# Optimization experiments

Measured on AMD Instinct MI355X. Metric: run time of the kernel, lower is better.

Reference implementation:

```python
import jax, jax.numpy as jnp
import numpy as np

N_VOX, N_COLS = 200000, 5   # (N, 1 + 3 coords + 1 feat)
N_CLUSTS, PTS_PER_CLUST = 1024, 128
N_EDGES = 8192


def setup_inputs() -> dict:
    key = jax.random.key(0)
    k1, k2, k3 = jax.random.split(key, 3)
    data = jax.random.normal(k1, (N_VOX, N_COLS), dtype=jnp.float32)
    clusts = jax.random.randint(k2, (N_CLUSTS, PTS_PER_CLUST), 0, N_VOX)
    edge_index = jax.random.randint(k3, (2, N_EDGES), 0, N_CLUSTS)
    return {"data": data, "clusts": clusts, "edge_index": edge_index}


def reference(data, clusts, edge_index):
    # COORD_COLS = columns 1:4 of the sparse tensor
    voxels = data[:, 1:4]                       # [N, 3]
    pts = voxels[clusts]                        # [C, P, 3]
    x1 = pts[edge_index[0]]                     # [E, P, 3] first cluster of each edge
    x2 = pts[edge_index[1]]                     # [E, P, 3] second cluster
    P = x1.shape[1]

    # per-edge pairwise squared distances (argmin of d^2 == argmin of d)
    d2 = jnp.sum((x1[:, :, None, :] - x2[:, None, :, :]) ** 2, axis=-1)  # [E, P, P]
    imin = jnp.argmin(d2.reshape(d2.shape[0], -1), axis=1)               # [E]
    i1, i2 = imin // P, imin % P

    v1 = jnp.take_along_axis(x1, i1[:, None, None], axis=1)[:, 0, :]     # [E, 3]
    v2 = jnp.take_along_axis(x2, i2[:, None, None], axis=1)[:, 0, :]     # [E, 3]

    disp = v1 - v2
    lend = jnp.linalg.norm(disp, axis=-1, keepdims=True)                 # [E, 1]
    safe = jnp.where(lend > 0, lend, 1.0)
    dispn = jnp.where(lend > 0, disp / safe, disp)                       # unit displacement

    B = (dispn[:, :, None] * dispn[:, None, :]).reshape(-1, 9)           # outer product, [E, 9]

    feats = jnp.concatenate([v1, v2, dispn, lend, B], axis=1)            # [E, 19]
    # undirected: interleave original and flipped (v1<->v2, disp -> -disp, B invariant)
    feats_flip = jnp.concatenate([v2, v1, -dispn, lend, B], axis=1)
    full = jnp.stack([feats, feats_flip], axis=1).reshape(-1, 19)        # [2E, 19]
    return full
```

## Files before the change

### kernel.cpp

```cpp
#include <hip/hip_runtime.h>
#include <cstdint>

#define NV 200000
#define NCOLS 5
#define P 128
#define NE 8192

__global__ __launch_bounds__(256) void clust_geo_edge_kernel(
    const float* __restrict__ data,
    const int*   __restrict__ clusts,
    const int*   __restrict__ edge_index,
    float*       __restrict__ out)
{
    const int e = blockIdx.x;
    const int t = threadIdx.x;

    __shared__ float x1s[P][3];
    __shared__ float x2s[P][3];
    __shared__ unsigned long long wmin[4];

    const int c1 = edge_index[e];
    const int c2 = edge_index[NE + e];

    if (t < P) {
        const int v = clusts[c1 * P + t];
        x1s[t][0] = data[v * NCOLS + 1];
        x1s[t][1] = data[v * NCOLS + 2];
        x1s[t][2] = data[v * NCOLS + 3];
    } else {
        const int p = t - P;
        const int v = clusts[c2 * P + p];
        x2s[p][0] = data[v * NCOLS + 1];
        x2s[p][1] = data[v * NCOLS + 2];
        x2s[p][2] = data[v * NCOLS + 3];
    }
    __syncthreads();

    const int i  = t >> 1;
    const int j0 = (t & 1) * 64;
    const float ax = x1s[i][0], ay = x1s[i][1], az = x1s[i][2];

    float bestd = __builtin_inff();
    int   bestflat = i * P + j0;

    #pragma unroll 8
    for (int k = 0; k < 64; ++k) {
        const int j = j0 + k;
        const float dx = __fsub_rn(ax, x2s[j][0]);
        const float dy = __fsub_rn(ay, x2s[j][1]);
        const float dz = __fsub_rn(az, x2s[j][2]);
        const float d2 = __fadd_rn(__fadd_rn(__fmul_rn(dx, dx), __fmul_rn(dy, dy)),
                                   __fmul_rn(dz, dz));
        if (d2 < bestd) { bestd = d2; bestflat = i * P + j; }
    }

    unsigned long long key =
        ((unsigned long long)__float_as_uint(bestd) << 32) | (unsigned)bestflat;

    for (int off = 32; off > 0; off >>= 1) {
        unsigned long long other = __shfl_down(key, off, 64);
        if (other < key) key = other;
    }
    const int wave = t >> 6;
    if ((t & 63) == 0) wmin[wave] = key;
    __syncthreads();

    if (t == 0) {
        unsigned long long k0 = wmin[0];
        #pragma unroll
        for (int w = 1; w < 4; ++w) if (wmin[w] < k0) k0 = wmin[w];
        const int flat = (int)(k0 & 0xffffffffull);
        const int i1 = flat >> 7;
        const int i2 = flat & (P - 1);

        const float v1x = x1s[i1][0], v1y = x1s[i1][1], v1z = x1s[i1][2];
        const float v2x = x2s[i2][0], v2y = x2s[i2][1], v2z = x2s[i2][2];

        const float dx = v1x - v2x, dy = v1y - v2y, dz = v1z - v2z;
        const float lend = sqrtf(dx * dx + dy * dy + dz * dz);

        float nx, ny, nz;
        if (lend > 0.f) { nx = dx / lend; ny = dy / lend; nz = dz / lend; }
        else            { nx = dx;        ny = dy;        nz = dz;        }

        const float B[9] = { nx*nx, nx*ny, nx*nz,
                             ny*nx, ny*ny, ny*nz,
                             nz*nx, nz*ny, nz*nz };

        float* o = out + (size_t)e * 38;
        o[0] = v1x; o[1] = v1y; o[2] = v1z;
        o[3] = v2x; o[4] = v2y; o[5] = v2z;
        o[6] = nx;  o[7] = ny;  o[8] = nz;  o[9] = lend;
        #pragma unroll
        for (int q = 0; q < 9; ++q) o[10 + q] = B[q];
        o[19] = v2x; o[20] = v2y; o[21] = v2z;
        o[22] = v1x; o[23] = v1y; o[24] = v1z;
        o[25] = -nx; o[26] = -ny; o[27] = -nz; o[28] = lend;
        #pragma unroll
        for (int q = 0; q < 9; ++q) o[29 + q] = B[q];
    }
}

extern "C" void kernel_launch(void* const* d_in, const int* in_sizes, int n_in,
                              void* d_out, int out_size, void* d_ws, size_t ws_size,
                              hipStream_t stream) {
    const float* data       = (const float*)d_in[0];
    const int*   clusts     = (const int*)d_in[1];
    const int*   edge_index = (const int*)d_in[2];
    float*       out        = (float*)d_out;

    clust_geo_edge_kernel<<<NE, 256, 0, stream>>>(data, clusts, edge_index, out);
}
```

Baseline: 98.08 us.

## Register-tile pairwise distance loop 8x8 per thread with float4 shared layout

Each thread now holds 8 points from each cluster in registers and computes an 8x8 block of distances, in place of streaming 64 points from shared memory against a single point. Cluster coordinates are stored padded to float4 so each point can be read from LDS with one vector load. This cuts LDS traffic per distance computation at the cost of more registers and a per-row argmin merge. Ties within a thread are still resolved by lowest flat index, since k increases with i and m increases with j.

```diff
diff --git a/kernel.cpp b/kernel.cpp
--- a/kernel.cpp
+++ b/kernel.cpp
@@ -15,8 +15,8 @@
     const int e = blockIdx.x;
     const int t = threadIdx.x;
 
-    __shared__ float x1s[P][3];
-    __shared__ float x2s[P][3];
+    __shared__ float4 x1s[P];
+    __shared__ float4 x2s[P];
     __shared__ unsigned long long wmin[4];
 
     const int c1 = edge_index[e];
@@ -24,34 +24,50 @@
 
     if (t < P) {
         const int v = clusts[c1 * P + t];
-        x1s[t][0] = data[v * NCOLS + 1];
-        x1s[t][1] = data[v * NCOLS + 2];
-        x1s[t][2] = data[v * NCOLS + 3];
+        x1s[t] = make_float4(data[v * NCOLS + 1], data[v * NCOLS + 2],
+                             data[v * NCOLS + 3], 0.f);
     } else {
         const int p = t - P;
         const int v = clusts[c2 * P + p];
-        x2s[p][0] = data[v * NCOLS + 1];
-        x2s[p][1] = data[v * NCOLS + 2];
-        x2s[p][2] = data[v * NCOLS + 3];
+        x2s[p] = make_float4(data[v * NCOLS + 1], data[v * NCOLS + 2],
+                             data[v * NCOLS + 3], 0.f);
     }
     __syncthreads();
 
-    const int i  = t >> 1;
-    const int j0 = (t & 1) * 64;
-    const float ax = x1s[i][0], ay = x1s[i][1], az = x1s[i][2];
+    const int tj = t & 15;
+    const int ti = t >> 4;
+
+    float4 a[8], b[8];
+    #pragma unroll
+    for (int k = 0; k < 8; ++k) a[k] = x1s[ti + 16 * k];
+    #pragma unroll
+    for (int m = 0; m < 8; ++m) b[m] = x2s[tj + 16 * m];
+
+    float bd[8];
+    int   bj[8];
+    #pragma unroll
+    for (int k = 0; k < 8; ++k) { bd[k] = __builtin_inff(); bj[k] = 0; }
+
+    #pragma unroll
+    for (int m = 0; m < 8; ++m) {
+        const int j = tj + 16 * m;
+        const float bx = b[m].x, by = b[m].y, bz = b[m].z;
+        #pragma unroll
+        for (int k = 0; k < 8; ++k) {
+            const float dx = __fsub_rn(a[k].x, bx);
+            const float dy = __fsub_rn(a[k].y, by);
+            const float dz = __fsub_rn(a[k].z, bz);
+            const float d2 = __fadd_rn(__fadd_rn(__fmul_rn(dx, dx), __fmul_rn(dy, dy)),
+                                       __fmul_rn(dz, dz));
+            if (d2 < bd[k]) { bd[k] = d2; bj[k] = j; }
+        }
+    }
 
     float bestd = __builtin_inff();
-    int   bestflat = i * P + j0;
-
-    #pragma unroll 8
-    for (int k = 0; k < 64; ++k) {
-        const int j = j0 + k;
-        const float dx = __fsub_rn(ax, x2s[j][0]);
-        const float dy = __fsub_rn(ay, x2s[j][1]);
-        const float dz = __fsub_rn(az, x2s[j][2]);
-        const float d2 = __fadd_rn(__fadd_rn(__fmul_rn(dx, dx), __fmul_rn(dy, dy)),
-                                   __fmul_rn(dz, dz));
-        if (d2 < bestd) { bestd = d2; bestflat = i * P + j; }
+    int   bestflat = 0;
+    #pragma unroll
+    for (int k = 0; k < 8; ++k) {
+        if (bd[k] < bestd) { bestd = bd[k]; bestflat = (ti + 16 * k) * P + bj[k]; }
     }
 
     unsigned long long key =
@@ -73,8 +89,8 @@
         const int i1 = flat >> 7;
         const int i2 = flat & (P - 1);
 
-        const float v1x = x1s[i1][0], v1y = x1s[i1][1], v1z = x1s[i1][2];
-        const float v2x = x2s[i2][0], v2y = x2s[i2][1], v2z = x2s[i2][2];
+        const float v1x = x1s[i1].x, v1y = x1s[i1].y, v1z = x1s[i1].z;
+        const float v2x = x2s[i2].x, v2y = x2s[i2].y, v2z = x2s[i2].z;
 
         const float dx = v1x - v2x, dy = v1y - v2y, dz = v1z - v2z;
         const float lend = sqrtf(dx * dx + dy * dy + dz * dz);
```

Result: faster. 94.53 us (-3.6%).
